# Performance work log

Hardware: AMD Instinct MI355X
Metric: run time of the kernel (lower is better)

The kernel has to match this reference:

```python
import jax, jax.numpy as jnp
import numpy as np
from jax import lax

B, CIN, H, W = 16, 96, 112, 112
C1, C2 = CIN * 2, CIN * 4          # 192, 384 (t1=(2,2))
SQ = 24                            # make_divisible(96//4, 4)
EPS = 1e-5


def _conv(x, w, stride, pad, groups):
    return lax.conv_general_dilated(
        x, w, window_strides=stride, padding=pad,
        feature_group_count=groups,
        dimension_numbers=("NCHW", "OIHW", "NCHW"))


def _bn(x, g, b, m, v):
    scale = (g / jnp.sqrt(v + EPS))[None, :, None, None]
    return (x - m[None, :, None, None]) * scale + b[None, :, None, None]


def _shuffle(x, groups):
    b, c, h, w = x.shape
    return x.reshape(b, groups, c // groups, h, w).transpose(0, 2, 1, 3, 4).reshape(b, c, h, w)


# DYShiftMax channel permutation for g=1: rotate channels left by 1
_DY_IDX = np.roll(np.arange(CIN), -1)


def setup_inputs() -> dict:
    key = jax.random.key(0)
    ks = jax.random.split(key, 16)
    f32 = jnp.float32
    d = {}
    d["x"] = jax.random.normal(ks[0], (B, CIN, H, W), f32)
    # depthwise (k,1) conv, groups=CIN, multiplier 2
    d["w_dw1"] = jax.random.normal(ks[1], (C1, 1, 3, 1), f32) * 0.2
    d["bn1_g"] = jax.random.uniform(ks[2], (C1,), f32, 0.5, 1.5)
    d["bn1_b"] = jax.random.normal(ks[3], (C1,), f32) * 0.1
    d["bn1_m"] = jax.random.normal(ks[4], (C1,), f32) * 0.1
    d["bn1_v"] = jax.random.uniform(ks[5], (C1,), f32, 0.5, 1.5)
    # depthwise (1,k) conv, groups=C1, multiplier 2
    d["w_dw2"] = jax.random.normal(ks[6], (C2, 1, 1, 3), f32) * 0.2
    d["bn2_g"] = jax.random.uniform(ks[7], (C2,), f32, 0.5, 1.5)
    d["bn2_b"] = jax.random.normal(ks[8], (C2,), f32) * 0.1
    d["bn2_m"] = jax.random.normal(ks[9], (C2,), f32) * 0.1
    d["bn2_v"] = jax.random.uniform(ks[10], (C2,), f32, 0.5, 1.5)
    # 1x1 pointwise conv 384 -> 96 (ConvModule, bias-free conv + BN, identity act)
    d["w_pw"] = jax.random.normal(ks[11], (CIN, C2, 1, 1), f32) * (1.0 / np.sqrt(C2))
    d["bn3_g"] = jax.random.uniform(ks[12], (CIN,), f32, 0.5, 1.5)
    d["bn3_b"] = jax.random.normal(ks[13], (CIN,), f32) * 0.1
    d["bn3_m"] = jax.random.normal(ks[14], (CIN,), f32) * 0.1
    d["bn3_v"] = jax.random.uniform(ks[15], (CIN,), f32, 0.5, 1.5)
    # DYShiftMax squeeze-excite FC: CIN -> SQ -> 2*CIN (exp=2)
    k2 = jax.random.split(jax.random.fold_in(key, 1), 4)
    d["fc1_w"] = jax.random.normal(k2[0], (SQ, CIN), f32) * (1.0 / np.sqrt(CIN))
    d["fc1_b"] = jax.random.normal(k2[1], (SQ,), f32) * 0.1
    d["fc2_w"] = jax.random.normal(k2[2], (2 * CIN, SQ), f32) * (1.0 / np.sqrt(SQ))
    d["fc2_b"] = jax.random.normal(k2[3], (2 * CIN,), f32) * 0.1
    return d


def reference(x, w_dw1, bn1_g, bn1_b, bn1_m, bn1_v,
              w_dw2, bn2_g, bn2_b, bn2_m, bn2_v,
              w_pw, bn3_g, bn3_b, bn3_m, bn3_v,
              fc1_w, fc1_b, fc2_w, fc2_b):
    # DepthSpatialSepConv: depthwise (3,1) then depthwise (1,3), each + BN
    h = _conv(x, w_dw1, (1, 1), ((1, 1), (0, 0)), groups=CIN)
    h = _bn(h, bn1_g, bn1_b, bn1_m, bn1_v)
    h = _conv(h, w_dw2, (1, 1), ((0, 0), (1, 1)), groups=C1)
    h = _bn(h, bn2_g, bn2_b, bn2_m, bn2_v)
    # ReLU6 (y2 == 0)
    h = jnp.clip(h, 0.0, 6.0)
    # ChannelShuffle(6)
    h = _shuffle(h, 6)
    # 1x1 ConvModule (groups=1, identity activation) + BN
    h = _conv(h, w_pw, (1, 1), ((0, 0), (0, 0)), groups=1)
    h = _bn(h, bn3_g, bn3_b, bn3_m, bn3_v)
    # DYShiftMax(out, out, (1,0), (0,0), act_relu=False -> exp=2, g=1)
    y = h.mean(axis=(2, 3))                       # [B, CIN] global avg pool
    y = jnp.maximum(y @ fc1_w.T + fc1_b, 0.0)     # Linear + ReLU
    y = y @ fc2_w.T + fc2_b                       # Linear -> [B, 2*CIN]
    y = jnp.clip(y + 3.0, 0.0, 6.0) / 6.0         # HSigmoid
    y = (y - 0.5) * 4.0
    a1 = y[:, :CIN] + 1.0                         # init_a[0] = 1.0
    b1 = y[:, CIN:]                               # init_b[0] = 0.0
    h2 = h[:, _DY_IDX, :, :]                      # shifted channels
    h = h * a1[:, :, None, None] + h2 * b1[:, :, None, None]
    # ChannelShuffle(g2=1) is identity; ChannelShuffle(out//2)
    h = _shuffle(h, CIN // 2)
    # residual (stride==1 and in==out)
    return h + x
```

## Files before the change

kernel.cpp:

```cpp
#include <hip/hip_runtime.h>
#include <hip/hip_bf16.h>

#define BATCH 16
#define CINC 96
#define HGT 112
#define WID 112
#define HW 12544
#define C1N 192
#define C2N 384
#define EPSV 1e-5f

typedef _Float16 f16x8 __attribute__((ext_vector_type(8)));
typedef _Float16 f16x4 __attribute__((ext_vector_type(4)));
typedef float    f32x4 __attribute__((ext_vector_type(4)));

#define WS_S      0
#define WS_A1B1   1536
#define WS_W1F    4608
#define WS_B1F    5184
#define WS_W2F    5376
#define WS_B2F    6528
#define WS_S3     6912
#define WS_B3     7008
#define WS_WPF_BYTES (7104*4)
#define WS_H_BYTES   (WS_WPF_BYTES + CINC*C2N*2)

__global__ void k_prep(const float* __restrict__ wdw1, const float* __restrict__ g1,
                       const float* __restrict__ bb1, const float* __restrict__ m1,
                       const float* __restrict__ v1,
                       const float* __restrict__ wdw2, const float* __restrict__ g2,
                       const float* __restrict__ bb2, const float* __restrict__ m2,
                       const float* __restrict__ v2,
                       const float* __restrict__ wpw, const float* __restrict__ g3,
                       const float* __restrict__ bb3, const float* __restrict__ m3,
                       const float* __restrict__ v3,
                       float* ws)
{
    int t = blockIdx.x * blockDim.x + threadIdx.x;
    int stride = gridDim.x * blockDim.x;
    float* w1f = ws + WS_W1F; float* b1f = ws + WS_B1F;
    float* w2f = ws + WS_W2F; float* b2f = ws + WS_B2F;
    float* s3  = ws + WS_S3;  float* b3f = ws + WS_B3;
    _Float16* wpf = (_Float16*)((char*)ws + WS_WPF_BYTES);

    for (int c = t; c < C1N; c += stride) {
        float s = g1[c] / sqrtf(v1[c] + EPSV);
        w1f[c*3+0] = wdw1[c*3+0] * s;
        w1f[c*3+1] = wdw1[c*3+1] * s;
        w1f[c*3+2] = wdw1[c*3+2] * s;
        b1f[c] = bb1[c] - m1[c] * s;
    }
    for (int c = t; c < C2N; c += stride) {
        float s = g2[c] / sqrtf(v2[c] + EPSV);
        w2f[c*3+0] = wdw2[c*3+0] * s;
        w2f[c*3+1] = wdw2[c*3+1] * s;
        w2f[c*3+2] = wdw2[c*3+2] * s;
        b2f[c] = bb2[c] - m2[c] * s;
    }
    for (int c = t; c < CINC; c += stride) {
        float s = g3[c] / sqrtf(v3[c] + EPSV);
        s3[c] = s; b3f[c] = bb3[c] - m3[c] * s;
    }
    for (int idx = t; idx < CINC * C2N; idx += stride) {
        int e = idx & 7;
        int l2 = idx >> 3;
        int lane = l2 & 63;
        int l3 = l2 >> 6;
        int rt = l3 % 6, ksg = l3 / 6;
        int m = rt * 16 + (lane & 15);
        int k = ksg * 32 + (lane >> 4) * 8 + e;
        int o = (k & 63) * 6 + (k >> 6);
        wpf[idx] = (_Float16)wpw[m * C2N + o];
    }
}

__global__ __launch_bounds__(256, 2) void k_main5(const float* __restrict__ x,
                                                  const float* __restrict__ ws,
                                                  float* __restrict__ sums,
                                                  _Float16* __restrict__ h_out)
{
    __shared__ __align__(16) char u_raw[256 * 208];
    __shared__ __align__(16) f16x8 wpf_s[1152];
    __shared__ float ssum[CINC];

    int t   = threadIdx.x;
    int bid = blockIdx.x;
    int logical = (bid & 7) * 112 + (bid >> 3);
    int b   = logical / 56;
    int rem = logical - b * 56;
    int y0  = (rem >> 1) * 4;
    int x0  = (rem & 1) * 48;

    int wv = t >> 6, lane = t & 63;
    int r = lane >> 4, c4 = lane & 15;
    int gy = y0 + r;
    int gc = x0 + 4 * c4;
    int col16 = c4, g = r;

    const float* w1f = ws + WS_W1F; const float* b1f = ws + WS_B1F;
    const float* w2f = ws + WS_W2F; const float* b2f = ws + WS_B2F;

    if (t < CINC) ssum[t] = 0.f;

    bool ymok = gy >= 1;
    bool ypok = gy + 1 < HGT;
    bool isE  = (c4 == 0) | (c4 == 15);
    int  ecol = (c4 == 0) ? (x0 - 1) : (x0 + 64);
    bool ev   = isE && ((unsigned)ecol < (unsigned)WID);
    int  secol = ev ? ecol : 0;
    int  tm = ymok ? -WID : 0;
    int  tp = ypok ?  WID : 0;

    f32x4 acc[6][4];
    #pragma unroll
    for (int rt = 0; rt < 6; ++rt)
        #pragma unroll
        for (int ct = 0; ct < 4; ++ct) acc[rt][ct] = (f32x4){0.f, 0.f, 0.f, 0.f};

    const f16x8* wpf_g = (const f16x8*)((const char*)ws + WS_WPF_BYTES);
    long xb = (long)b * CINC * HW;
    long rowoff = (long)gy * WID;

    for (int chunk = 0; chunk < 4; ++chunk) {
        if (chunk) __syncthreads();

        #pragma unroll
        for (int j = 0; j < 5; ++j) {
            int idx = t + j * 256;
            if (idx < 1152) wpf_s[idx] = wpf_g[chunk * 1152 + idx];
        }

        #pragma unroll 2
        for (int i = 0; i < 6; ++i) {
            int cl = wv * 6 + i;
            int cu = __builtin_amdgcn_readfirstlane(chunk * 24 + cl);
            const float* xc = x + xb + (long)cu * HW;
            const float* xp = xc + rowoff + gc;
            f32x4 mid = *(const f32x4*)xp;
            f32x4 top = *(const f32x4*)(xp + tm);
            f32x4 bot = *(const f32x4*)(xp + tp);

            float eT = 0.f, eM = 0.f, eB = 0.f;
            if (isE) {
                const float* ep = xc + rowoff + secol;
                eM = ep[0];
                eT = ep[tm];
                eB = ep[tp];
            }

            int c1a = cu * 2;
            float wa0 = w1f[c1a*3+0], wa1 = w1f[c1a*3+1], wa2 = w1f[c1a*3+2], ba = b1f[c1a];
            float wb0 = w1f[c1a*3+3], wb1 = w1f[c1a*3+4], wb2 = w1f[c1a*3+5], bb = b1f[c1a+1];

            float va[4], vb[4];
            #pragma unroll
            for (int j = 0; j < 4; ++j) {
                float tt = ymok ? top[j] : 0.f;
                float bt = ypok ? bot[j] : 0.f;
                va[j] = fmaf(wa0, tt, fmaf(wa1, mid[j], fmaf(wa2, bt, ba)));
                vb[j] = fmaf(wb0, tt, fmaf(wb1, mid[j], fmaf(wb2, bt, bb)));
            }
            float etS = (ymok && ev) ? eT : 0.f;
            float ebS = (ypok && ev) ? eB : 0.f;
            float emS = ev ? eM : 0.f;
            float vea = ev ? fmaf(wa0, etS, fmaf(wa1, emS, fmaf(wa2, ebS, ba))) : 0.f;
            float veb = ev ? fmaf(wb0, etS, fmaf(wb1, emS, fmaf(wb2, ebS, bb))) : 0.f;

            float vLa = __shfl(va[3], (lane + 63) & 63);
            float vLb = __shfl(vb[3], (lane + 63) & 63);
            float vRa = __shfl(va[0], (lane + 1) & 63);
            float vRb = __shfl(vb[0], (lane + 1) & 63);
            if (c4 == 0)  { vLa = vea; vLb = veb; }
            if (c4 == 15) { vRa = vea; vRb = veb; }

            int c2b = cu * 4;
            float w20[4], w21[4], w22[4], b2v[4];
            #pragma unroll
            for (int jj = 0; jj < 4; ++jj) {
                w20[jj] = w2f[(c2b+jj)*3+0];
                w21[jj] = w2f[(c2b+jj)*3+1];
                w22[jj] = w2f[(c2b+jj)*3+2];
                b2v[jj] = b2f[c2b+jj];
            }

            float pa[6] = {vLa, va[0], va[1], va[2], va[3], vRa};
            float pb[6] = {vLb, vb[0], vb[1], vb[2], vb[3], vRb};
            int slot = ((cl >> 1) + 3 * r + c4) % 12;
            int off8 = (cl & 1) * 8;
            char* ubase = u_raw + (r * 64 + 4 * c4) * 208 + slot * 16 + off8;
            #pragma unroll
            for (int j = 0; j < 4; ++j) {
                f16x4 uv;
                #pragma unroll
                for (int jj = 0; jj < 4; ++jj) {
                    float p0 = (jj < 2) ? pa[j]     : pb[j];
                    float p1 = (jj < 2) ? pa[j + 1] : pb[j + 1];
                    float p2 = (jj < 2) ? pa[j + 2] : pb[j + 2];
                    float tv = fmaf(w20[jj], p0, fmaf(w21[jj], p1, fmaf(w22[jj], p2, b2v[jj])));
                    tv = fminf(fmaxf(tv, 0.f), 6.f);
                    uv[jj] = (_Float16)tv;
                }
                *(f16x4*)(ubase + j * 208) = uv;
            }
        }
        __syncthreads();

        #pragma unroll
        for (int ks = 0; ks < 3; ++ks) {
            f16x8 bfr[4];
            #pragma unroll
            for (int ct = 0; ct < 4; ++ct) {
                int pos = wv * 64 + ct * 16 + col16;
                int sl = (ks * 4 + g + 3 * wv + ((pos >> 2) & 15)) % 12;
                bfr[ct] = *(const f16x8*)(u_raw + pos * 208 + sl * 16);
            }
            #pragma unroll
            for (int rt = 0; rt < 6; ++rt) {
                f16x8 afr = wpf_s[(ks * 6 + rt) * 64 + lane];
                #pragma unroll
                for (int ct = 0; ct < 4; ++ct)
                    acc[rt][ct] = __builtin_amdgcn_mfma_f32_16x16x32_f16(afr, bfr[ct], acc[rt][ct], 0, 0, 0);
            }
        }
    }
    __syncthreads();

    _Float16* h_s = (_Float16*)u_raw;
    const float* s3  = ws + WS_S3;
    const float* b3f = ws + WS_B3;
    #pragma unroll
    for (int rt = 0; rt < 6; ++rt) {
        #pragma unroll
        for (int ct = 0; ct < 4; ++ct) {
            int p = wv * 64 + ct * 16 + col16;
            #pragma unroll
            for (int rr = 0; rr < 4; ++rr) {
                int m = rt * 16 + g * 4 + rr;
                h_s[m * 264 + p] = (_Float16)fmaf(acc[rt][ct][rr], s3[m], b3f[m]);
            }
        }
    }
    __syncthreads();

    #pragma unroll
    for (int i = 0; i < 12; ++i) {
        int flat = i * 2048 + t * 8;
        int m = flat >> 8;
        int p = flat & 255;
        f16x8 hv = *(const f16x8*)(h_s + m * 264 + p);
        int row = y0 + (p >> 6);
        int colg = x0 + (p & 63);
        *(f16x8*)(h_out + ((long)(b * CINC + m)) * HW + (long)row * WID + colg) = hv;

        float s = 0.f;
        if (!(x0 == 48 && (p & 63) < 16)) {
            #pragma unroll
            for (int e = 0; e < 8; ++e) s += (float)hv[e];
        }
        s += __shfl_xor(s, 1);
        s += __shfl_xor(s, 2);
        s += __shfl_xor(s, 4);
        s += __shfl_xor(s, 8);
        s += __shfl_xor(s, 16);
        if ((lane & 31) == 0) atomicAdd(&ssum[m], s);
    }
    __syncthreads();
    if (t < CINC) atomicAdd(&sums[b * CINC + t], ssum[t]);
}

__global__ __launch_bounds__(192) void k_gates(const float* __restrict__ sums,
                                               const float* __restrict__ fc1w,
                                               const float* __restrict__ fc1b,
                                               const float* __restrict__ fc2w,
                                               const float* __restrict__ fc2b,
                                               float* __restrict__ a1b1)
{
    __shared__ float mean_s[CINC];
    __shared__ float mid[24];
    int b = blockIdx.x;
    int t = threadIdx.x;

    if (t < CINC) mean_s[t] = sums[b * CINC + t] * (1.0f / 12544.0f);
    __syncthreads();
    if (t < 24) {
        float d = fc1b[t];
        #pragma unroll 4
        for (int c = 0; c < CINC; ++c) d = fmaf(fc1w[t * CINC + c], mean_s[c], d);
        mid[t] = fmaxf(d, 0.f);
    }
    __syncthreads();
    {
        float d = fc2b[t];
        #pragma unroll
        for (int j = 0; j < 24; ++j) d = fmaf(fc2w[t * 24 + j], mid[j], d);
        float y = fminf(fmaxf(d + 3.f, 0.f), 6.f) * (1.f / 6.f);
        y = (y - 0.5f) * 4.f;
        a1b1[b * 192 + t] = (t < CINC) ? (y + 1.f) : y;
    }
}

__global__ __launch_bounds__(256) void k_final(const _Float16* __restrict__ h,
                                               const float* __restrict__ xin,
                                               const float* __restrict__ a1b1,
                                               float* __restrict__ out)
{
    int q = blockIdx.x * 256 + threadIdx.x;
    int pos4 = q % 3136;
    int bo = q / 3136;
    int o = bo % CINC, b = bo / CINC;
    int c = (o % 48) * 2 + (o / 48);
    int cn = (c + 1) % CINC;

    float av = a1b1[b * 192 + c];
    float bv = a1b1[b * 192 + 96 + c];

    long hb = (long)b * CINC * HW;
    f16x4 hv4 = *(const f16x4*)(h + hb + (long)c  * HW + pos4 * 4);
    f16x4 h2v = *(const f16x4*)(h + hb + (long)cn * HW + pos4 * 4);

    long xo = ((long)(b * CINC + o)) * HW + pos4 * 4;
    f32x4 xv = *(const f32x4*)(xin + xo);
    f32x4 rr;
    #pragma unroll
    for (int j = 0; j < 4; ++j)
        rr[j] = fmaf((float)hv4[j], av, fmaf((float)h2v[j], bv, xv[j]));
    *(f32x4*)(out + xo) = rr;
}

extern "C" void kernel_launch(void* const* d_in, const int* in_sizes, int n_in,
                              void* d_out, int out_size, void* d_ws, size_t ws_size,
                              hipStream_t stream)
{
    const float* x    = (const float*)d_in[0];
    const float* wdw1 = (const float*)d_in[1];
    const float* g1   = (const float*)d_in[2];
    const float* b1   = (const float*)d_in[3];
    const float* m1   = (const float*)d_in[4];
    const float* v1   = (const float*)d_in[5];
    const float* wdw2 = (const float*)d_in[6];
    const float* g2   = (const float*)d_in[7];
    const float* b2   = (const float*)d_in[8];
    const float* m2   = (const float*)d_in[9];
    const float* v2   = (const float*)d_in[10];
    const float* wpw  = (const float*)d_in[11];
    const float* g3   = (const float*)d_in[12];
    const float* b3   = (const float*)d_in[13];
    const float* m3   = (const float*)d_in[14];
    const float* v3   = (const float*)d_in[15];
    const float* fc1w = (const float*)d_in[16];
    const float* fc1b = (const float*)d_in[17];
    const float* fc2w = (const float*)d_in[18];
    const float* fc2b = (const float*)d_in[19];

    float* ws   = (float*)d_ws;
    float* sums = ws + WS_S;
    float* a1b1 = ws + WS_A1B1;
    _Float16* hbuf = (_Float16*)((char*)d_ws + WS_H_BYTES);
    float* out  = (float*)d_out;

    hipMemsetAsync(sums, 0, 1536 * sizeof(float), stream);
    k_prep<<<dim3(40), dim3(256), 0, stream>>>(
        wdw1, g1, b1, m1, v1, wdw2, g2, b2, m2, v2,
        wpw, g3, b3, m3, v3, ws);
    k_main5<<<dim3(896), dim3(256), 0, stream>>>(x, ws, sums, hbuf);
    k_gates<<<dim3(BATCH), dim3(192), 0, stream>>>(sums, fc1w, fc1b, fc2w, fc2b, a1b1);
    k_final<<<dim3(4816896 / 256), dim3(256), 0, stream>>>(hbuf, x, a1b1, out);
}
```

Baseline: 120.1 us.

## Drop LDS weight staging, pair channel stores, raise occupancy target to three

The pointwise weight fragments are now read straight from global memory (via cache) inside the MFMA loop instead of being staged in shared memory each chunk. This removes a per-chunk copy and shrinks LDS use, allowing the launch bound to ask for three blocks per SM. Consecutive channel pairs are buffered in registers and written to LDS as one 16-byte store instead of two 8-byte stores. The trade-off is global-load latency on the A fragments during the MFMA loop and more register pressure from the full unroll under a tighter register budget.

```diff
diff --git a/kernel.cpp b/kernel.cpp
--- a/kernel.cpp
+++ b/kernel.cpp
@@ -74,13 +74,12 @@
     }
 }
 
-__global__ __launch_bounds__(256, 2) void k_main5(const float* __restrict__ x,
+__global__ __launch_bounds__(256, 3) void k_main6(const float* __restrict__ x,
                                                   const float* __restrict__ ws,
                                                   float* __restrict__ sums,
                                                   _Float16* __restrict__ h_out)
 {
     __shared__ __align__(16) char u_raw[256 * 208];
-    __shared__ __align__(16) f16x8 wpf_s[1152];
     __shared__ float ssum[CINC];
 
     int t   = threadIdx.x;
@@ -121,16 +120,14 @@
     long xb = (long)b * CINC * HW;
     long rowoff = (long)gy * WID;
 
+    int rotbase = 3 * r + c4;
+    char* ub0 = u_raw + (r * 64 + 4 * c4) * 208;
+
     for (int chunk = 0; chunk < 4; ++chunk) {
         if (chunk) __syncthreads();
 
-        #pragma unroll
-        for (int j = 0; j < 5; ++j) {
-            int idx = t + j * 256;
-            if (idx < 1152) wpf_s[idx] = wpf_g[chunk * 1152 + idx];
-        }
-
-        #pragma unroll 2
+        f16x4 uvbuf[4];
+        #pragma unroll
         for (int i = 0; i < 6; ++i) {
             int cl = wv * 6 + i;
             int cu = __builtin_amdgcn_readfirstlane(chunk * 24 + cl);
@@ -185,12 +182,10 @@
 
             float pa[6] = {vLa, va[0], va[1], va[2], va[3], vRa};
             float pb[6] = {vLb, vb[0], vb[1], vb[2], vb[3], vRb};
-            int slot = ((cl >> 1) + 3 * r + c4) % 12;
-            int off8 = (cl & 1) * 8;
-            char* ubase = u_raw + (r * 64 + 4 * c4) * 208 + slot * 16 + off8;
+
+            f16x4 uv[4];
             #pragma unroll
             for (int j = 0; j < 4; ++j) {
-                f16x4 uv;
                 #pragma unroll
                 for (int jj = 0; jj < 4; ++jj) {
                     float p0 = (jj < 2) ? pa[j]     : pb[j];
@@ -198,9 +193,21 @@
                     float p2 = (jj < 2) ? pa[j + 2] : pb[j + 2];
                     float tv = fmaf(w20[jj], p0, fmaf(w21[jj], p1, fmaf(w22[jj], p2, b2v[jj])));
                     tv = fminf(fmaxf(tv, 0.f), 6.f);
-                    uv[jj] = (_Float16)tv;
+                    uv[j][jj] = (_Float16)tv;
                 }
-                *(f16x4*)(ubase + j * 208) = uv;
+            }
+
+            if ((i & 1) == 0) {
+                #pragma unroll
+                for (int j = 0; j < 4; ++j) uvbuf[j] = uv[j];
+            } else {
+                int slot = ((cl >> 1) + rotbase) % 12;
+                char* ubase = ub0 + slot * 16;
+                #pragma unroll
+                for (int j = 0; j < 4; ++j) {
+                    f16x8 w = __builtin_shufflevector(uvbuf[j], uv[j], 0, 1, 2, 3, 4, 5, 6, 7);
+                    *(f16x8*)(ubase + j * 208) = w;
+                }
             }
         }
         __syncthreads();
@@ -216,7 +223,7 @@
             }
             #pragma unroll
             for (int rt = 0; rt < 6; ++rt) {
-                f16x8 afr = wpf_s[(ks * 6 + rt) * 64 + lane];
+                f16x8 afr = wpf_g[((chunk * 3 + ks) * 6 + rt) * 64 + lane];
                 #pragma unroll
                 for (int ct = 0; ct < 4; ++ct)
                     acc[rt][ct] = __builtin_amdgcn_mfma_f32_16x16x32_f16(afr, bfr[ct], acc[rt][ct], 0, 0, 0);
@@ -362,7 +369,7 @@
     k_prep<<<dim3(40), dim3(256), 0, stream>>>(
         wdw1, g1, b1, m1, v1, wdw2, g2, b2, m2, v2,
         wpw, g3, b3, m3, v3, ws);
-    k_main5<<<dim3(896), dim3(256), 0, stream>>>(x, ws, sums, hbuf);
+    k_main6<<<dim3(896), dim3(256), 0, stream>>>(x, ws, sums, hbuf);
     k_gates<<<dim3(BATCH), dim3(192), 0, stream>>>(sums, fc1w, fc1b, fc2w, fc2b, a1b1);
     k_final<<<dim3(4816896 / 256), dim3(256), 0, stream>>>(hbuf, x, a1b1, out);
 }
```

Result: slower. 134.5 us (+12.0%).
